# Optimization experiments

Measured on AMD Instinct MI355X. Metric: run time of the kernel, lower is better.

## Reference

```python
import jax, jax.numpy as jnp
import numpy as np
import math

D_MODEL, N_HEADS, N_LEVELS, N_POINTS = 256, 8, 4, 4
SPATIAL = [(80, 80), (40, 40), (20, 20), (10, 10)]


def setup_inputs() -> dict:
    key = jax.random.key(0)
    ks = jax.random.split(key, 8)
    N = 1
    C, H, L, P = D_MODEL, N_HEADS, N_LEVELS, N_POINTS
    shapes = np.array(SPATIAL, np.int32)
    len_in = int((shapes[:, 0] * shapes[:, 1]).sum())  # 8500
    Lq = len_in  # encoder self-attention: queries == flattened pixels
    start = np.concatenate([[0], np.cumsum(shapes[:, 0] * shapes[:, 1])[:-1]]).astype(np.int32)

    query = jax.random.normal(ks[0], (N, Lq, C), jnp.float32)
    reference_points = jax.random.uniform(ks[1], (N, Lq, L, 2), dtype=jnp.float32)
    input_flatten = jax.random.normal(ks[2], (N, len_in, C), jnp.float32)

    # sampling_offsets bias: grid init as in _reset_parameters
    thetas = jnp.arange(H, dtype=jnp.float32) * (2.0 * math.pi / H)
    grid = jnp.stack([jnp.cos(thetas), jnp.sin(thetas)], -1)
    grid = grid / jnp.max(jnp.abs(grid), axis=-1, keepdims=True)
    grid = jnp.tile(grid[:, None, None, :], (1, L, P, 1)) * jnp.arange(1, P + 1, dtype=jnp.float32)[None, None, :, None]
    b_off = grid.reshape(-1)
    W_off = jax.random.normal(ks[3], (C, H * L * P * 2), jnp.float32) * 0.01
    W_attn = jax.random.normal(ks[4], (C, H * L * P), jnp.float32) * 0.01
    b_attn = jnp.zeros((H * L * P,), jnp.float32)
    s = 1.0 / np.sqrt(C)
    W_v = jax.random.normal(ks[5], (C, C), jnp.float32) * s
    b_v = jnp.zeros((C,), jnp.float32)
    W_out = jax.random.normal(ks[6], (C, C), jnp.float32) * s
    b_out = jnp.zeros((C,), jnp.float32)
    return {
        "query": query, "reference_points": reference_points, "input_flatten": input_flatten,
        "input_spatial_shapes": jnp.asarray(shapes), "input_level_start_index": jnp.asarray(start),
        "W_off": W_off, "b_off": b_off, "W_attn": W_attn, "b_attn": b_attn,
        "W_v": W_v, "b_v": b_v, "W_out": W_out, "b_out": b_out,
    }


def _ms_deform_core(value, spatial_shapes, level_start_index, loc, attn):
    # value: (N, Len_in, H, d); loc: (N, Lq, H, L, P, 2) normalized [0,1]; attn: (N, Lq, H, L, P)
    N, Len_in, H, d = value.shape
    _, Lq, _, L, P, _ = loc.shape
    Hi = spatial_shapes[:, 0][None, None, None, :, None]  # (1,1,1,L,1)
    Wi = spatial_shapes[:, 1][None, None, None, :, None]
    # grid_sample(align_corners=False) semantics used by the CUDA ms_deform_attn kernel
    x = loc[..., 0] * Wi.astype(loc.dtype) - 0.5  # (N,Lq,H,L,P)
    y = loc[..., 1] * Hi.astype(loc.dtype) - 0.5
    x0 = jnp.floor(x); y0 = jnp.floor(y)
    lw = x - x0; lh = y - y0
    x0i = x0.astype(jnp.int32); y0i = y0.astype(jnp.int32)
    v = value.transpose(0, 2, 1, 3)  # (N,H,Len_in,d)
    start = level_start_index[None, None, None, :, None]
    out = jnp.zeros((N, Lq, H, d), value.dtype)
    corners = [(0, 0, (1 - lh) * (1 - lw)), (0, 1, (1 - lh) * lw),
               (1, 0, lh * (1 - lw)), (1, 1, lh * lw)]
    for dy, dx, wgt in corners:
        hc = y0i + dy; wc = x0i + dx
        valid = (hc >= 0) & (hc < Hi) & (wc >= 0) & (wc < Wi)
        idx = start + jnp.clip(hc, 0, Hi - 1) * Wi + jnp.clip(wc, 0, Wi - 1)  # (N,Lq,H,L,P)
        w = jnp.where(valid, wgt, 0.0) * attn  # (N,Lq,H,L,P)
        idx_g = idx.transpose(0, 2, 1, 3, 4).reshape(N, H, Lq * L * P)
        sampled = jnp.take_along_axis(v, idx_g[..., None], axis=2)  # (N,H,Lq*L*P,d)
        sampled = sampled.reshape(N, H, Lq, L, P, d)
        out = out + jnp.einsum('nhqlpd,nqhlp->nqhd', sampled, w)
    return out.reshape(N, Lq, H * d)


def reference(query, reference_points, input_flatten, input_spatial_shapes, input_level_start_index,
              W_off, b_off, W_attn, b_attn, W_v, b_v, W_out, b_out):
    N, Lq, C = query.shape
    H, L, P = N_HEADS, N_LEVELS, N_POINTS
    d = C // H
    value = (input_flatten @ W_v + b_v).reshape(N, -1, H, d)
    off = (query @ W_off + b_off).reshape(N, Lq, H, L, P, 2)
    attn = jax.nn.softmax((query @ W_attn + b_attn).reshape(N, Lq, H, L * P), axis=-1)
    attn = attn.reshape(N, Lq, H, L, P)
    # reference_points last dim == 2 branch
    norm = jnp.stack([input_spatial_shapes[:, 1], input_spatial_shapes[:, 0]], -1).astype(query.dtype)  # (L,2) = (W,H)
    loc = reference_points[:, :, None, :, None, :] + off / norm[None, None, None, :, None, :]
    out = _ms_deform_core(value, input_spatial_shapes, input_level_start_index, loc, attn)
    return out @ W_out + b_out
```

## Files before the change

### kernel.cpp

```cpp
#include <hip/hip_runtime.h>

#define LQ    8500
#define C_DIM 256

typedef __attribute__((ext_vector_type(8))) short bf16x8;
typedef __attribute__((ext_vector_type(4))) float f32x4;

__device__ __forceinline__ unsigned short f2bf(float x) {
    union { float f; unsigned u; } c; c.f = x;
    unsigned r = c.u + 0x7FFFu + ((c.u >> 16) & 1u);
    return (unsigned short)(r >> 16);
}
__device__ __forceinline__ float bf2f(unsigned us) {
    union { unsigned u; float f; } c; c.u = us << 16;
    return c.f;
}

__device__ __forceinline__ void gload_lds16(const void* g, void* l) {
    __builtin_amdgcn_global_load_lds(
        (const __attribute__((address_space(1))) unsigned int*)g,
        (__attribute__((address_space(3))) unsigned int*)l, 16, 0, 0);
}

__global__ __launch_bounds__(256)
void prep_w(const float* __restrict__ Wv,   const float* __restrict__ Wout,
            const float* __restrict__ Woff, const float* __restrict__ Wattn,
            const float* __restrict__ boff, const float* __restrict__ battn,
            unsigned short* __restrict__ Wv_t, unsigned short* __restrict__ Wout_t,
            unsigned short* __restrict__ Wcat_t, float* __restrict__ bcat)
{
    const int total = 65536 * 3 + 32768 + 384;
    for (int i = blockIdx.x * 256 + threadIdx.x; i < total; i += gridDim.x * 256) {
        if (i < 65536) {
            int k = i >> 8, n = i & 255;
            Wv_t[n * 256 + k] = f2bf(Wv[i]);
        } else if (i < 131072) {
            int j = i - 65536; int k = j >> 8, n = j & 255;
            Wout_t[n * 256 + k] = f2bf(Wout[j]);
        } else if (i < 196608) {
            int j = i - 131072; int k = j >> 8, n = j & 255;
            Wcat_t[n * 256 + k] = f2bf(Woff[j]);
        } else if (i < 229376) {
            int j = i - 196608; int k = j >> 7, n = j & 127;
            Wcat_t[(256 + n) * 256 + k] = f2bf(Wattn[j]);
        } else {
            int j = i - 229376;
            bcat[j] = (j < 256) ? boff[j] : battn[j - 256];
        }
    }
}

template<int OUTMODE, bool A_F32>
__device__ __forceinline__ void gemm_body(
    const void* __restrict__ Av, const unsigned short* __restrict__ Bt,
    const float* __restrict__ bias, void* __restrict__ Out,
    int M, int N, int r0, int c0,
    char* As, char* Bs)
{
    const int t    = threadIdx.x;
    const int lane = t & 63, wave = t >> 6;
    const int wr   = wave >> 1, wc = wave & 1;
    const int lrow = lane & 15, lgrp = lane >> 4;

    f32x4 acc[2][2] = {{{}, {}}, {{}, {}}};
    float4 fa[2][2];

    auto loadA = [&](int buf, int k0) {
#pragma unroll
        for (int r = 0; r < 2; ++r) {
            const int rr = r * 32 + (t >> 3);
            if constexpr (A_F32) {
                const float* g = (const float*)Av +
                                 (size_t)min(r0 + rr, M - 1) * 256 + k0 + (t & 7) * 8;
                fa[r][0] = ((const float4*)g)[0];
                fa[r][1] = ((const float4*)g)[1];
            } else {
                const int chunk = (t & 7) ^ (rr & 7);
                const unsigned short* g = (const unsigned short*)Av +
                                          (size_t)min(r0 + rr, M - 1) * 256 + k0 + chunk * 8;
                gload_lds16(g, As + buf * 8192 + r * 4096 + wave * 1024);
            }
        }
    };
    auto writeA = [&](int buf) {
        if constexpr (A_F32) {
#pragma unroll
            for (int r = 0; r < 2; ++r) {
                const int rr = r * 32 + (t >> 3);
                bf16x8 o;
                o[0] = (short)f2bf(fa[r][0].x); o[1] = (short)f2bf(fa[r][0].y);
                o[2] = (short)f2bf(fa[r][0].z); o[3] = (short)f2bf(fa[r][0].w);
                o[4] = (short)f2bf(fa[r][1].x); o[5] = (short)f2bf(fa[r][1].y);
                o[6] = (short)f2bf(fa[r][1].z); o[7] = (short)f2bf(fa[r][1].w);
                *(bf16x8*)(As + buf * 8192 + rr * 128 +
                           (((t & 7) ^ (rr & 7)) * 16)) = o;
            }
        }
    };
    auto loadB = [&](int buf, int k0) {
#pragma unroll
        for (int r = 0; r < 2; ++r) {
            const int rr = r * 32 + (t >> 3);
            const int chunk = (t & 7) ^ (rr & 7);
            const unsigned short* g = Bt + (size_t)(c0 + rr) * 256 + k0 + chunk * 8;
            gload_lds16(g, Bs + buf * 8192 + r * 4096 + wave * 1024);
        }
    };

    auto compute = [&](int buf) {
#pragma unroll
        for (int kk = 0; kk < 2; ++kk) {
            const int g = kk * 4 + lgrp;
            bf16x8 a[2], b[2];
#pragma unroll
            for (int mi = 0; mi < 2; ++mi) {
                const int row = wr * 32 + mi * 16 + lrow;
                a[mi] = *(const bf16x8*)(As + buf * 8192 + row * 128 +
                                         ((g ^ (row & 7)) * 16));
            }
#pragma unroll
            for (int nj = 0; nj < 2; ++nj) {
                const int row = wc * 32 + nj * 16 + lrow;
                b[nj] = *(const bf16x8*)(Bs + buf * 8192 + row * 128 +
                                         ((g ^ (row & 7)) * 16));
            }
#pragma unroll
            for (int mi = 0; mi < 2; ++mi)
#pragma unroll
                for (int nj = 0; nj < 2; ++nj)
                    acc[mi][nj] = __builtin_amdgcn_mfma_f32_16x16x32_bf16(
                        a[mi], b[nj], acc[mi][nj], 0, 0, 0);
        }
    };

    loadA(0, 0); loadB(0, 0); writeA(0);
    __syncthreads();
    int cur = 0;
#pragma unroll
    for (int it = 0; it < 3; ++it) {
        loadA(cur ^ 1, (it + 1) * 64);
        loadB(cur ^ 1, (it + 1) * 64);
        compute(cur);
        writeA(cur ^ 1);
        __syncthreads();
        cur ^= 1;
    }
    compute(cur);

#pragma unroll
    for (int mi = 0; mi < 2; ++mi)
#pragma unroll
        for (int nj = 0; nj < 2; ++nj) {
            const int col = c0 + wc * 32 + nj * 16 + lrow;
            const float bb = bias[col];
#pragma unroll
            for (int j = 0; j < 4; ++j) {
                const int row = r0 + wr * 32 + mi * 16 + lgrp * 4 + j;
                if (row < M) {
                    const float v = acc[mi][nj][j] + bb;
                    if constexpr (OUTMODE == 0)
                        ((float*)Out)[(size_t)row * N + col] = v;
                    else if constexpr (OUTMODE == 1)
                        ((unsigned short*)Out)[(size_t)row * N + col] = f2bf(v);
                    else
                        ((unsigned short*)Out)[(size_t)(col >> 5) * (LQ * 32) +
                                               (size_t)row * 32 + (col & 31)] = f2bf(v);
                }
            }
        }
}

__global__ __launch_bounds__(256)
void gemm_dual(const float* __restrict__ A0, const unsigned short* __restrict__ B0,
               const float* __restrict__ bias0, unsigned short* __restrict__ out0,
               const float* __restrict__ A1, const unsigned short* __restrict__ B1,
               const float* __restrict__ bias1, unsigned short* __restrict__ out1)
{
    __shared__ __align__(16) char As[2 * 64 * 64 * 2];
    __shared__ __align__(16) char Bs[2 * 64 * 64 * 2];
    const int y  = blockIdx.y;
    const int r0 = blockIdx.x * 64;
    if (y < 4)
        gemm_body<2, true>(A0, B0, bias0, out0, LQ, 256, r0, y * 64, As, Bs);
    else
        gemm_body<1, true>(A1, B1, bias1, out1, LQ, 384, r0, (y - 4) * 64, As, Bs);
}

__global__ __launch_bounds__(256)
void gemm_f32out(const unsigned short* __restrict__ A, const unsigned short* __restrict__ Bt,
                 const float* __restrict__ bias, float* __restrict__ out)
{
    __shared__ __align__(16) char As[2 * 64 * 64 * 2];
    __shared__ __align__(16) char Bs[2 * 64 * 64 * 2];
    gemm_body<0, false>(A, Bt, bias, out, LQ, 256, blockIdx.x * 64, blockIdx.y * 64,
                        As, Bs);
}

__global__ __launch_bounds__(256)
void msda_sample(const unsigned short* __restrict__ value,
                 const unsigned short* __restrict__ offattn,
                 const float* __restrict__ refp,
                 const int*   __restrict__ shapes,
                 const int*   __restrict__ lstart,
                 unsigned short* __restrict__ msda)
{
    __shared__ int   s_off[2][128][5];
    __shared__ float s_w[2][128][5];

    const int t   = threadIdx.x;
    const int sub = t >> 7, tl = t & 127;
    const int q   = blockIdx.x * 2 + sub;

    {
        const int lp = tl & 15, l = lp >> 2;
        const int Hs = shapes[2 * l + 0];
        const int Ws = shapes[2 * l + 1];
        const int st = lstart[l];

        const unsigned oxy = *(const unsigned*)(offattn + (size_t)q * 384 + 2 * tl);
        const float ox = bf2f(oxy & 0xffffu);
        const float oy = bf2f(oxy >> 16);
        const float rx = refp[q * 8 + l * 2 + 0];
        const float ry = refp[q * 8 + l * 2 + 1];

        const float x = (rx + ox / (float)Ws) * (float)Ws - 0.5f;
        const float y = (ry + oy / (float)Hs) * (float)Hs - 0.5f;
        const float x0f = floorf(x), y0f = floorf(y);
        const float lw = x - x0f, lh = y - y0f;
        const int   x0 = (int)x0f, y0 = (int)y0f;

        const float logit = bf2f(offattn[(size_t)q * 384 + 256 + tl]);
        float m = logit;
        for (int s = 8; s >= 1; s >>= 1) m = fmaxf(m, __shfl_xor(m, s, 16));
        const float e = __expf(logit - m);
        float ssum = e;
        for (int s = 8; s >= 1; s >>= 1) ssum += __shfl_xor(ssum, s, 16);
        const float a = e / ssum;

#pragma unroll
        for (int corner = 0; corner < 4; ++corner) {
            const int dy = corner >> 1, dx = corner & 1;
            const int hc = y0 + dy, wc = x0 + dx;
            const bool valid = (hc >= 0) && (hc < Hs) && (wc >= 0) && (wc < Ws);
            const float wy = dy ? lh : (1.f - lh);
            const float wx = dx ? lw : (1.f - lw);
            const int hcc = min(max(hc, 0), Hs - 1);
            const int wcc = min(max(wc, 0), Ws - 1);
            s_off[sub][tl][corner] = (st + hcc * Ws + wcc) * 64;
            s_w[sub][tl][corner]   = valid ? (wy * wx * a) : 0.f;
        }
    }
    __syncthreads();

    const int chunk = tl & 3, quarter = (tl >> 2) & 3, h = tl >> 4;
    const char* vb = (const char*)value + (size_t)h * (LQ * 64) + chunk * 16;
    float a0 = 0.f, a1 = 0.f, a2 = 0.f, a3 = 0.f;
    float a4 = 0.f, a5 = 0.f, a6 = 0.f, a7 = 0.f;
#pragma unroll
    for (int j = 0; j < 4; ++j) {
        const int c = h * 16 + quarter * 4 + j;
#pragma unroll
        for (int corner = 0; corner < 4; ++corner) {
            const float w  = s_w[sub][c][corner];
            const int   bo = s_off[sub][c][corner];
            const uint4 v = *(const uint4*)(vb + (size_t)(unsigned)bo);
            a0 = fmaf(w, bf2f(v.x & 0xffffu), a0);
            a1 = fmaf(w, bf2f(v.x >> 16), a1);
            a2 = fmaf(w, bf2f(v.y & 0xffffu), a2);
            a3 = fmaf(w, bf2f(v.y >> 16), a3);
            a4 = fmaf(w, bf2f(v.z & 0xffffu), a4);
            a5 = fmaf(w, bf2f(v.z >> 16), a5);
            a6 = fmaf(w, bf2f(v.w & 0xffffu), a6);
            a7 = fmaf(w, bf2f(v.w >> 16), a7);
        }
    }
    a0 += __shfl_xor(a0, 4); a0 += __shfl_xor(a0, 8);
    a1 += __shfl_xor(a1, 4); a1 += __shfl_xor(a1, 8);
    a2 += __shfl_xor(a2, 4); a2 += __shfl_xor(a2, 8);
    a3 += __shfl_xor(a3, 4); a3 += __shfl_xor(a3, 8);
    a4 += __shfl_xor(a4, 4); a4 += __shfl_xor(a4, 8);
    a5 += __shfl_xor(a5, 4); a5 += __shfl_xor(a5, 8);
    a6 += __shfl_xor(a6, 4); a6 += __shfl_xor(a6, 8);
    a7 += __shfl_xor(a7, 4); a7 += __shfl_xor(a7, 8);
    if (quarter == 0) {
        uint4 o;
        o.x = (unsigned)f2bf(a0) | ((unsigned)f2bf(a1) << 16);
        o.y = (unsigned)f2bf(a2) | ((unsigned)f2bf(a3) << 16);
        o.z = (unsigned)f2bf(a4) | ((unsigned)f2bf(a5) << 16);
        o.w = (unsigned)f2bf(a6) | ((unsigned)f2bf(a7) << 16);
        *(uint4*)(msda + (size_t)q * 256 + h * 32 + chunk * 8) = o;
    }
}

extern "C" void kernel_launch(void* const* d_in, const int* in_sizes, int n_in,
                              void* d_out, int out_size, void* d_ws, size_t ws_size,
                              hipStream_t stream)
{
    const float* query  = (const float*)d_in[0];
    const float* refp   = (const float*)d_in[1];
    const float* inflat = (const float*)d_in[2];
    const int*   shapes = (const int*)  d_in[3];
    const int*   lstart = (const int*)  d_in[4];
    const float* W_off  = (const float*)d_in[5];
    const float* b_off  = (const float*)d_in[6];
    const float* W_attn = (const float*)d_in[7];
    const float* b_attn = (const float*)d_in[8];
    const float* W_v    = (const float*)d_in[9];
    const float* b_v    = (const float*)d_in[10];
    const float* W_out  = (const float*)d_in[11];
    const float* b_out  = (const float*)d_in[12];

    float* out = (float*)d_out;
    char*  ws  = (char*)d_ws;

    size_t o = 0;
    unsigned short* Wv_t   = (unsigned short*)(ws + o); o += 131072;
    unsigned short* Wout_t = (unsigned short*)(ws + o); o += 131072;
    unsigned short* Wcat_t = (unsigned short*)(ws + o); o += 196608;
    float*          bcat   = (float*)         (ws + o); o += 1536;
    unsigned short* value  = (unsigned short*)(ws + o); o += (size_t)LQ * 256 * 2;
    unsigned short* offattn= (unsigned short*)(ws + o); o += (size_t)LQ * 384 * 2;
    unsigned short* msda   = (unsigned short*)(ws + o);

    prep_w<<<128, 256, 0, stream>>>(W_v, W_out, W_off, W_attn, b_off, b_attn,
                                    Wv_t, Wout_t, Wcat_t, bcat);

    gemm_dual<<<dim3(133, 10), 256, 0, stream>>>(inflat, Wv_t, b_v, value,
                                                 query, Wcat_t, bcat, offattn);

    msda_sample<<<4250, 256, 0, stream>>>(value, offattn, refp, shapes, lstart, msda);

    gemm_f32out<<<dim3(133, 4), 256, 0, stream>>>(msda, Wout_t, b_out, out);
}
```

Before: 58.28 us.

## Stage fp32 A tiles via direct-to-LDS loads and remap sampler blocks per XCD

The fp32-input GEMM now loads A tiles straight into LDS as fp32 with global_load_lds and a 16-chunk XOR swizzle, converting to bf16 at fragment-read time. This drops the register round-trip and the separate writeA step, at the cost of twice the LDS for A and repeated conversions inside the inner loop. The sampling kernel remaps block IDs so each XCD handles a contiguous range of queries, which should improve L2 locality for value gathers. prep_w also launches twice as many blocks.

```diff
diff --git a/kernel.cpp b/kernel.cpp
--- a/kernel.cpp
+++ b/kernel.cpp
@@ -5,6 +5,7 @@
 
 typedef __attribute__((ext_vector_type(8))) short bf16x8;
 typedef __attribute__((ext_vector_type(4))) float f32x4;
+typedef __attribute__((ext_vector_type(8))) __bf16 bf8v;
 
 __device__ __forceinline__ unsigned short f2bf(float x) {
     union { float f; unsigned u; } c; c.f = x;
@@ -14,6 +15,16 @@
 __device__ __forceinline__ float bf2f(unsigned us) {
     union { unsigned u; float f; } c; c.u = us << 16;
     return c.f;
+}
+
+__device__ __forceinline__ bf16x8 cvt8(f32x4 lo, f32x4 hi) {
+    bf8v b;
+    b[0] = (__bf16)lo[0]; b[1] = (__bf16)lo[1];
+    b[2] = (__bf16)lo[2]; b[3] = (__bf16)lo[3];
+    b[4] = (__bf16)hi[0]; b[5] = (__bf16)hi[1];
+    b[6] = (__bf16)hi[2]; b[7] = (__bf16)hi[3];
+    union { bf8v b; bf16x8 s; } u; u.b = b;
+    return u.s;
 }
 
 __device__ __forceinline__ void gload_lds16(const void* g, void* l) {
@@ -50,7 +61,7 @@
     }
 }
 
-template<int OUTMODE, bool A_F32>
+template<int OUTMODE, bool AF32>
 __device__ __forceinline__ void gemm_body(
     const void* __restrict__ Av, const unsigned short* __restrict__ Bt,
     const float* __restrict__ bias, void* __restrict__ Out,
@@ -61,48 +72,35 @@
     const int lane = t & 63, wave = t >> 6;
     const int wr   = wave >> 1, wc = wave & 1;
     const int lrow = lane & 15, lgrp = lane >> 4;
+    constexpr int ABUF = AF32 ? 16384 : 8192;
 
     f32x4 acc[2][2] = {{{}, {}}, {{}, {}}};
-    float4 fa[2][2];
-
-    auto loadA = [&](int buf, int k0) {
+
+    auto stage = [&](int buf, int k0) {
+        if constexpr (AF32) {
+#pragma unroll
+            for (int r = 0; r < 4; ++r) {
+                const int row = r * 16 + (t >> 4);
+                const int c16 = (t & 15) ^ (row & 15);
+                const float* g = (const float*)Av +
+                                 (size_t)min(r0 + row, M - 1) * 256 + k0 + c16 * 4;
+                gload_lds16(g, As + buf * ABUF + r * 4096 + wave * 1024);
+            }
+        } else {
+#pragma unroll
+            for (int r = 0; r < 2; ++r) {
+                const int row   = r * 32 + (t >> 3);
+                const int chunk = (t & 7) ^ (row & 7);
+                const unsigned short* g = (const unsigned short*)Av +
+                    (size_t)min(r0 + row, M - 1) * 256 + k0 + chunk * 8;
+                gload_lds16(g, As + buf * ABUF + r * 4096 + wave * 1024);
+            }
+        }
 #pragma unroll
         for (int r = 0; r < 2; ++r) {
-            const int rr = r * 32 + (t >> 3);
-            if constexpr (A_F32) {
-                const float* g = (const float*)Av +
-                                 (size_t)min(r0 + rr, M - 1) * 256 + k0 + (t & 7) * 8;
-                fa[r][0] = ((const float4*)g)[0];
-                fa[r][1] = ((const float4*)g)[1];
-            } else {
-                const int chunk = (t & 7) ^ (rr & 7);
-                const unsigned short* g = (const unsigned short*)Av +
-                                          (size_t)min(r0 + rr, M - 1) * 256 + k0 + chunk * 8;
-                gload_lds16(g, As + buf * 8192 + r * 4096 + wave * 1024);
-            }
-        }
-    };
-    auto writeA = [&](int buf) {
-        if constexpr (A_F32) {
-#pragma unroll
-            for (int r = 0; r < 2; ++r) {
-                const int rr = r * 32 + (t >> 3);
-                bf16x8 o;
-                o[0] = (short)f2bf(fa[r][0].x); o[1] = (short)f2bf(fa[r][0].y);
-                o[2] = (short)f2bf(fa[r][0].z); o[3] = (short)f2bf(fa[r][0].w);
-                o[4] = (short)f2bf(fa[r][1].x); o[5] = (short)f2bf(fa[r][1].y);
-                o[6] = (short)f2bf(fa[r][1].z); o[7] = (short)f2bf(fa[r][1].w);
-                *(bf16x8*)(As + buf * 8192 + rr * 128 +
-                           (((t & 7) ^ (rr & 7)) * 16)) = o;
-            }
-        }
-    };
-    auto loadB = [&](int buf, int k0) {
-#pragma unroll
-        for (int r = 0; r < 2; ++r) {
-            const int rr = r * 32 + (t >> 3);
-            const int chunk = (t & 7) ^ (rr & 7);
-            const unsigned short* g = Bt + (size_t)(c0 + rr) * 256 + k0 + chunk * 8;
+            const int row   = r * 32 + (t >> 3);
+            const int chunk = (t & 7) ^ (row & 7);
+            const unsigned short* g = Bt + (size_t)(c0 + row) * 256 + k0 + chunk * 8;
             gload_lds16(g, Bs + buf * 8192 + r * 4096 + wave * 1024);
         }
     };
@@ -115,8 +113,15 @@
 #pragma unroll
             for (int mi = 0; mi < 2; ++mi) {
                 const int row = wr * 32 + mi * 16 + lrow;
-                a[mi] = *(const bf16x8*)(As + buf * 8192 + row * 128 +
-                                         ((g ^ (row & 7)) * 16));
+                if constexpr (AF32) {
+                    const char* base = As + buf * ABUF + row * 256;
+                    const f32x4 lo = *(const f32x4*)(base + (((2*g+0) ^ (row & 15)) * 16));
+                    const f32x4 hi = *(const f32x4*)(base + (((2*g+1) ^ (row & 15)) * 16));
+                    a[mi] = cvt8(lo, hi);
+                } else {
+                    a[mi] = *(const bf16x8*)(As + buf * ABUF + row * 128 +
+                                             ((g ^ (row & 7)) * 16));
+                }
             }
 #pragma unroll
             for (int nj = 0; nj < 2; ++nj) {
@@ -133,15 +138,13 @@
         }
     };
 
-    loadA(0, 0); loadB(0, 0); writeA(0);
+    stage(0, 0);
     __syncthreads();
     int cur = 0;
 #pragma unroll
     for (int it = 0; it < 3; ++it) {
-        loadA(cur ^ 1, (it + 1) * 64);
-        loadB(cur ^ 1, (it + 1) * 64);
+        stage(cur ^ 1, (it + 1) * 64);
         compute(cur);
-        writeA(cur ^ 1);
         __syncthreads();
         cur ^= 1;
     }
@@ -176,8 +179,8 @@
                const float* __restrict__ A1, const unsigned short* __restrict__ B1,
                const float* __restrict__ bias1, unsigned short* __restrict__ out1)
 {
-    __shared__ __align__(16) char As[2 * 64 * 64 * 2];
-    __shared__ __align__(16) char Bs[2 * 64 * 64 * 2];
+    __shared__ __align__(16) char As[2 * 64 * 256];
+    __shared__ __align__(16) char Bs[2 * 64 * 128];
     const int y  = blockIdx.y;
     const int r0 = blockIdx.x * 64;
     if (y < 4)
@@ -190,8 +193,8 @@
 void gemm_f32out(const unsigned short* __restrict__ A, const unsigned short* __restrict__ Bt,
                  const float* __restrict__ bias, float* __restrict__ out)
 {
-    __shared__ __align__(16) char As[2 * 64 * 64 * 2];
-    __shared__ __align__(16) char Bs[2 * 64 * 64 * 2];
+    __shared__ __align__(16) char As[2 * 64 * 128];
+    __shared__ __align__(16) char Bs[2 * 64 * 128];
     gemm_body<0, false>(A, Bt, bias, out, LQ, 256, blockIdx.x * 64, blockIdx.y * 64,
                         As, Bs);
 }
@@ -207,9 +210,13 @@
     __shared__ int   s_off[2][128][5];
     __shared__ float s_w[2][128][5];
 
+    const int orig = blockIdx.x;
+    const int xcd  = orig & 7, pos = orig >> 3;
+    const int wgid = (xcd < 2 ? xcd * 532 : 1064 + (xcd - 2) * 531) + pos;
+
     const int t   = threadIdx.x;
     const int sub = t >> 7, tl = t & 127;
-    const int q   = blockIdx.x * 2 + sub;
+    const int q   = wgid * 2 + sub;
 
     {
         const int lp = tl & 15, l = lp >> 2;
@@ -322,7 +329,7 @@
     unsigned short* offattn= (unsigned short*)(ws + o); o += (size_t)LQ * 384 * 2;
     unsigned short* msda   = (unsigned short*)(ws + o);
 
-    prep_w<<<128, 256, 0, stream>>>(W_v, W_out, W_off, W_attn, b_off, b_attn,
+    prep_w<<<256, 256, 0, stream>>>(W_v, W_out, W_off, W_attn, b_off, b_attn,
                                     Wv_t, Wout_t, Wcat_t, bcat);
 
     gemm_dual<<<dim3(133, 10), 256, 0, stream>>>(inflat, Wv_t, b_v, value,
```

After: 59.38 us. Within noise of the previous version (+1.9%).
